# Kernel tuning notes

Measured on AMD Instinct MI355X. Metric: run time of the kernel, lower is better.

Reference implementation:

```python
import jax, jax.numpy as jnp
from jax import lax
import numpy as np

B, T, IN, H, OUT = 64, 512, 128, 512, 1


def _lstm_layer(x, W_ih, W_hh, b_ih, b_hh):
    # x: [B, T, in]; W_ih: [4H, in]; W_hh: [4H, H]; biases: [4H]
    # PyTorch gate order: i, f, g, o
    xg = jnp.einsum('bti,gi->btg', x, W_ih) + (b_ih + b_hh)  # [B, T, 4H]
    Hd = W_hh.shape[1]
    h0 = jnp.zeros((x.shape[0], Hd), x.dtype)

    def step(carry, xt):
        h, c = carry
        g = xt + h @ W_hh.T  # [B, 4H]
        i, f, gg, o = jnp.split(g, 4, axis=-1)
        i = jax.nn.sigmoid(i)
        f = jax.nn.sigmoid(f)
        gg = jnp.tanh(gg)
        o = jax.nn.sigmoid(o)
        c = f * c + i * gg
        h = o * jnp.tanh(c)
        return (h, c), h

    (_, _), hs = lax.scan(step, (h0, h0), jnp.swapaxes(xg, 0, 1))  # hs: [T, B, H]
    return jnp.swapaxes(hs, 0, 1)  # [B, T, H]


def setup_inputs() -> dict:
    key = jax.random.key(0)
    ks = jax.random.split(key, 11)
    s_in = 1.0 / np.sqrt(H)
    inp = {
        'x': jax.random.normal(ks[0], (B, T, IN), jnp.float32),
        'W_ih0': jax.random.uniform(ks[1], (4 * H, IN), jnp.float32, -s_in, s_in),
        'W_hh0': jax.random.uniform(ks[2], (4 * H, H), jnp.float32, -s_in, s_in),
        'b_ih0': jax.random.uniform(ks[3], (4 * H,), jnp.float32, -s_in, s_in),
        'b_hh0': jax.random.uniform(ks[4], (4 * H,), jnp.float32, -s_in, s_in),
        'W_ih1': jax.random.uniform(ks[5], (4 * H, H), jnp.float32, -s_in, s_in),
        'W_hh1': jax.random.uniform(ks[6], (4 * H, H), jnp.float32, -s_in, s_in),
        'b_ih1': jax.random.uniform(ks[7], (4 * H,), jnp.float32, -s_in, s_in),
        'b_hh1': jax.random.uniform(ks[8], (4 * H,), jnp.float32, -s_in, s_in),
        'Wl': jax.random.uniform(ks[9], (OUT, H), jnp.float32, -s_in, s_in),
        'bl': jax.random.uniform(ks[10], (OUT,), jnp.float32, -s_in, s_in),
    }
    return inp


def reference(x, W_ih0, W_hh0, b_ih0, b_hh0, W_ih1, W_hh1, b_ih1, b_hh1, Wl, bl):
    h = _lstm_layer(x, W_ih0, W_hh0, b_ih0, b_hh0)   # layer 0
    h = _lstm_layer(h, W_ih1, W_hh1, b_ih1, b_hh1)   # layer 1
    last = h[:, -1, :]                                # [B, H]
    out = last @ Wl.T + bl                            # [B, OUT]; classification=False -> no sigmoid
    return out
```

## Files before the change

kernel.cpp:

```cpp
#include <hip/hip_runtime.h>
#include <cmath>

#define TT 512
#define BB 64
#define HH 512
#define II 128
#define NBLK 256

typedef float v2f __attribute__((ext_vector_type(2)));
__device__ __forceinline__ v2f fma2(v2f a, v2f b, v2f c) { return __builtin_elementwise_fma(a, b, c); }

#define SMEM_FLOATS (16384 + 16384 + 1024 + 256 + 16)
#define SMEM_BYTES  (SMEM_FLOATS * 4)

__device__ __forceinline__ float sigm(float v) { return 1.0f / (1.0f + expf(-v)); }
__device__ __forceinline__ unsigned umin2(unsigned a, unsigned b) { return a < b ? a : b; }
#define CBAR() asm volatile("" ::: "memory")

__device__ __forceinline__ v2f loadh2(const float* p) {
  unsigned long long r = __hip_atomic_load((const unsigned long long*)p,
                                           __ATOMIC_RELAXED, __HIP_MEMORY_SCOPE_AGENT);
  v2f v;
  v.x = __uint_as_float((unsigned)r);
  v.y = __uint_as_float((unsigned)(r >> 32));
  return v;
}
template<int KN>
__device__ __forceinline__ void loadh2b(const float* __restrict__ src, int k0,
                                        int bp, v2f (&v)[KN]) {
#pragma unroll
  for (int i = 0; i < KN; ++i) v[i] = loadh2(src + (size_t)(k0 + i) * BB + 2 * bp);
}
template<int KN>
__device__ __forceinline__ void loadx2(const float* __restrict__ src, int k0,
                                       int bp, v2f (&v)[KN]) {
#pragma unroll
  for (int i = 0; i < KN; ++i)
    v[i] = *(const v2f*)(src + (size_t)(k0 + i) * BB + 2 * bp);
}

__device__ __forceinline__ void step2(const float* wk8, v2f h2, v2f (&acc)[8]) {
  const float4* wp = (const float4*)wk8;
  const float4 w0 = wp[0], w1 = wp[1];
  acc[0] = fma2((v2f){w0.x, w0.x}, h2, acc[0]);
  acc[1] = fma2((v2f){w0.y, w0.y}, h2, acc[1]);
  acc[2] = fma2((v2f){w0.z, w0.z}, h2, acc[2]);
  acc[3] = fma2((v2f){w0.w, w0.w}, h2, acc[3]);
  acc[4] = fma2((v2f){w1.x, w1.x}, h2, acc[4]);
  acc[5] = fma2((v2f){w1.y, w1.y}, h2, acc[5]);
  acc[6] = fma2((v2f){w1.z, w1.z}, h2, acc[6]);
  acc[7] = fma2((v2f){w1.w, w1.w}, h2, acc[7]);
}
template<int KN>
__device__ __forceinline__ void consume2(const float* __restrict__ wro, int k0,
                                         const v2f (&v)[KN], v2f (&acc)[8]) {
#pragma unroll
  for (int i = 0; i < KN; ++i) step2(wro + (size_t)(k0 + i) * 16, v[i], acc);
}

__device__ __forceinline__ void span32(const float* __restrict__ src,
                                       const float* __restrict__ wro,
                                       int k0, int bp, v2f (&acc)[8]) {
  v2f a[4], b[4];
  loadh2b<4>(src, k0,      bp, a);
  loadh2b<4>(src, k0 + 4,  bp, b);
  consume2<4>(wro, k0,      a, acc);
  loadh2b<4>(src, k0 + 8,  bp, a);
  consume2<4>(wro, k0 + 4,  b, acc);
  loadh2b<4>(src, k0 + 12, bp, b);
  consume2<4>(wro, k0 + 8,  a, acc);
  loadh2b<4>(src, k0 + 16, bp, a);
  consume2<4>(wro, k0 + 12, b, acc);
  loadh2b<4>(src, k0 + 20, bp, b);
  consume2<4>(wro, k0 + 16, a, acc);
  loadh2b<4>(src, k0 + 24, bp, a);
  consume2<4>(wro, k0 + 20, b, acc);
  loadh2b<4>(src, k0 + 28, bp, b);
  consume2<4>(wro, k0 + 24, a, acc);
  consume2<4>(wro, k0 + 28, b, acc);
}

__global__ __launch_bounds__(1024) void k_transpose_x(const float* __restrict__ x,
                                                      float* __restrict__ xT) {
  __shared__ float tile[64][65];
  const int t  = blockIdx.x >> 1;
  const int k0 = (blockIdx.x & 1) << 6;
  const int lk = threadIdx.x & 63;
  const int lb = threadIdx.x >> 6;
#pragma unroll
  for (int bp = 0; bp < 64; bp += 16) {
    const int b = bp + lb;
    tile[lk][b] = x[((size_t)b * TT + t) * II + k0 + lk];
  }
  __syncthreads();
  const int b2  = threadIdx.x & 63;
  const int kk0 = threadIdx.x >> 6;
#pragma unroll
  for (int kp = 0; kp < 64; kp += 16) {
    const int kk = kp + kk0;
    xT[((size_t)t * II + k0 + kk) * BB + b2] = tile[kk][b2];
  }
}

__global__ void k_init_flags(unsigned* flags) { flags[threadIdx.x] = 0u; }

__global__ __launch_bounds__(1024, 4) void k_lstm_persist(
    const float* __restrict__ xT,
    const float* __restrict__ W_ih0, const float* __restrict__ W_hh0,
    const float* __restrict__ b_ih0, const float* __restrict__ b_hh0,
    const float* __restrict__ W_ih1, const float* __restrict__ W_hh1,
    const float* __restrict__ b_ih1, const float* __restrict__ b_hh1,
    float* __restrict__ h0ring, float* __restrict__ h1ring,
    unsigned* __restrict__ flags)
{
  extern __shared__ float smem[];
  float* wlds  = smem;
  float* part  = wlds + 16384;
  float* gates = part + 16384;
  float* cst   = gates + 1024;
  float* bsum  = cst + 256;

  const int bid = blockIdx.x;
  const int L   = bid >> 7;
  const int ub  = (bid & 127) << 2;
  const int tid = threadIdx.x;

  const float* WA = L ? W_ih1 : W_ih0;
  const float* WB = L ? W_hh1 : W_hh0;
  const int KA = L ? HH : II;

  const int ktot = KA + HH;
  for (int idx = tid; idx < 16 * ktot; idx += 1024) {
    const int k  = idx >> 4;
    const int lr = idx & 15;
    const int u = lr >> 2, q = lr & 3;
    const int G = q * HH + ub + u;
    wlds[idx] = (k < KA) ? WA[G * KA + k] : WB[G * HH + (k - KA)];
  }
  if (tid < 16) {
    const int u = tid >> 2, q = tid & 3;
    const int G = q * HH + ub + u;
    bsum[tid] = L ? (b_ih1[G] + b_hh1[G]) : (b_ih0[G] + b_hh0[G]);
  }
  if (tid < 256) cst[tid] = 0.0f;
  __syncthreads();

  const int bp    = tid & 31;
  const int rhalf = (tid >> 5) & 1;
  const int kseg  = tid >> 6;

  const float* wroA = wlds + rhalf * 8;
  const float* wroB0 = wlds + (size_t)II * 16 + rhalf * 8;
  const float* wroB1 = wlds + (size_t)HH * 16 + rhalf * 8;

  for (int s = 0; s <= TT; ++s) {
    const int t = L ? (s - 1) : s;
    const bool active = (t >= 0 && t < TT);
    const bool first  = (t == 0);

    v2f acc[8];
#pragma unroll
    for (int j = 0; j < 8; ++j) acc[j] = (v2f){0.0f, 0.0f};

    v2f xa[4], xb[4];
    if (active && L == 0) {
      const float* xp = xT + (size_t)t * (II * BB);
      loadx2<4>(xp, kseg * 8,     bp, xa);
      loadx2<4>(xp, kseg * 8 + 4, bp, xb);
    }

    if (s > 0) {
      if (tid < 64) {
        const unsigned tgt = (unsigned)s;
        for (;;) {
          const unsigned m0 = __hip_atomic_load(flags + tid,       __ATOMIC_RELAXED, __HIP_MEMORY_SCOPE_AGENT);
          const unsigned m1 = __hip_atomic_load(flags + tid +  64, __ATOMIC_RELAXED, __HIP_MEMORY_SCOPE_AGENT);
          const unsigned m2 = __hip_atomic_load(flags + tid + 128, __ATOMIC_RELAXED, __HIP_MEMORY_SCOPE_AGENT);
          const unsigned m3 = __hip_atomic_load(flags + tid + 192, __ATOMIC_RELAXED, __HIP_MEMORY_SCOPE_AGENT);
          const unsigned mn = umin2(umin2(m0, m1), umin2(m2, m3));
          if (__all(mn >= tgt)) break;
          __builtin_amdgcn_s_sleep(1);
        }
      }
      __syncthreads();
      CBAR();
    }

    if (active) {
      if (L == 0) {
        consume2<4>(wroA, kseg * 8,     xa, acc);
        consume2<4>(wroA, kseg * 8 + 4, xb, acc);
        if (!first) {
          span32(h0ring + (size_t)((s - 1) & 1) * (HH * BB),
                 wroB0, kseg * 32, bp, acc);
        }
      } else {
        span32(h0ring + (size_t)((s - 1) & 1) * (HH * BB),
               wroA, kseg * 32, bp, acc);
        if (!first) {
          span32(h1ring + (size_t)(s & 1) * (HH * BB),
                 wroB1, kseg * 32, bp, acc);
        }
      }

#pragma unroll
      for (int j = 0; j < 8; ++j) {
        const int row = rhalf * 8 + j;
        *(v2f*)(part + ((((size_t)row * 16 + kseg) * 32 + bp) << 1)) = acc[j];
      }
      __syncthreads();
      {
        const int row = tid >> 6;
        const int bb  = tid & 63;
        float g = 0.0f;
#pragma unroll
        for (int ks = 0; ks < 16; ++ks)
          g += part[((((size_t)row * 16 + ks) * 32 + (bb >> 1)) << 1) + (bb & 1)];
        gates[row * 64 + bb] = g + bsum[row];
      }
      __syncthreads();

      if (tid < 256) {
        const int u = tid >> 6, bb = tid & 63;
        const float gi = sigm(gates[((u << 2) + 0) * 64 + bb]);
        const float gf = sigm(gates[((u << 2) + 1) * 64 + bb]);
        const float gg = tanhf(gates[((u << 2) + 2) * 64 + bb]);
        const float go = sigm(gates[((u << 2) + 3) * 64 + bb]);
        const float cold = first ? 0.0f : cst[u * 64 + bb];
        const float cn = gf * cold + gi * gg;
        const float hn = go * tanhf(cn);
        cst[u * 64 + bb] = cn;
        float* hdst = (L ? h1ring : h0ring) + (size_t)(t & 1) * (HH * BB);
        float old = __hip_atomic_exchange(hdst + (ub + u) * 64 + bb, hn,
                                          __ATOMIC_RELAXED, __HIP_MEMORY_SCOPE_AGENT);
        asm volatile("" :: "v"(old));
      }
    }

    __syncthreads();
    if (tid == 0) {
      __hip_atomic_store(flags + bid, (unsigned)(s + 1),
                         __ATOMIC_RELAXED, __HIP_MEMORY_SCOPE_AGENT);
    }
  }
}

__global__ __launch_bounds__(512) void k_final(const float* __restrict__ h1last,
                                               const float* __restrict__ Wl,
                                               const float* __restrict__ bl,
                                               float* __restrict__ out) {
  __shared__ float red[8][64];
  const int jg = threadIdx.x >> 6, b = threadIdx.x & 63;
  float a = 0.0f;
  for (int jj = 0; jj < 64; ++jj) {
    const int j = (jg << 6) + jj;
    a += h1last[j * BB + b] * Wl[j];
  }
  red[jg][b] = a;
  __syncthreads();
  if (threadIdx.x < 64) {
    float s = bl[0];
#pragma unroll
    for (int g = 0; g < 8; ++g) s += red[g][threadIdx.x];
    out[threadIdx.x] = s;
  }
}

extern "C" void kernel_launch(void* const* d_in, const int* in_sizes, int n_in,
                              void* d_out, int out_size, void* d_ws, size_t ws_size,
                              hipStream_t stream) {
  (void)in_sizes; (void)n_in; (void)out_size; (void)ws_size;
  const float* x     = (const float*)d_in[0];
  const float* W_ih0 = (const float*)d_in[1];
  const float* W_hh0 = (const float*)d_in[2];
  const float* b_ih0 = (const float*)d_in[3];
  const float* b_hh0 = (const float*)d_in[4];
  const float* W_ih1 = (const float*)d_in[5];
  const float* W_hh1 = (const float*)d_in[6];
  const float* b_ih1 = (const float*)d_in[7];
  const float* b_hh1 = (const float*)d_in[8];
  const float* Wl    = (const float*)d_in[9];
  const float* bl    = (const float*)d_in[10];
  float* out = (float*)d_out;

  float* ws       = (float*)d_ws;
  float* xT       = ws;
  float* h0ring   = xT + (size_t)TT * II * BB;
  float* h1ring   = h0ring + 2 * HH * BB;
  unsigned* flags = (unsigned*)(h1ring + 2 * HH * BB);

  k_transpose_x<<<1024, 1024, 0, stream>>>(x, xT);
  k_init_flags<<<1, NBLK, 0, stream>>>(flags);

  hipFuncSetAttribute((const void*)k_lstm_persist,
                      hipFuncAttributeMaxDynamicSharedMemorySize, SMEM_BYTES);

  void* args[] = {
    (void*)&xT,
    (void*)&W_ih0, (void*)&W_hh0, (void*)&b_ih0, (void*)&b_hh0,
    (void*)&W_ih1, (void*)&W_hh1, (void*)&b_ih1, (void*)&b_hh1,
    (void*)&h0ring, (void*)&h1ring, (void*)&flags,
  };
  hipLaunchCooperativeKernel((void*)k_lstm_persist, dim3(NBLK), dim3(1024),
                             args, SMEM_BYTES, stream);

  k_final<<<1, 512, 0, stream>>>(h1ring + HH * BB, Wl, bl, out);
}
```

Before: 7.434 ms.

## Overlap input projection with flag spin, fast gate math, packed flag and h exchanges

Moves the layer-0 input-projection FMAs ahead of the inter-block flag wait so they overlap with synchronisation latency. Replaces expf/tanhf with hardware v_exp/v_rcp approximations and applies the activations during the gate reduction, spread over all 1024 threads instead of 256. The flag poll uses 64-bit loads (two flags each), h stores are packed as 64-bit atomic exchanges, and the final flag store is skipped. The fast approximations trade some accuracy, and the final flag skip relies on no consumer waiting for it.

```diff
diff --git a/kernel.cpp b/kernel.cpp
--- a/kernel.cpp
+++ b/kernel.cpp
@@ -13,7 +13,11 @@
 #define SMEM_FLOATS (16384 + 16384 + 1024 + 256 + 16)
 #define SMEM_BYTES  (SMEM_FLOATS * 4)
 
-__device__ __forceinline__ float sigm(float v) { return 1.0f / (1.0f + expf(-v)); }
+__device__ __forceinline__ float fexp2(float x) { float r; asm("v_exp_f32 %0, %1" : "=v"(r) : "v"(x)); return r; }
+__device__ __forceinline__ float frcpf(float x) { float r; asm("v_rcp_f32 %0, %1" : "=v"(r) : "v"(x)); return r; }
+__device__ __forceinline__ float sigm(float v)  { return frcpf(1.0f + fexp2(-1.44269504f * v)); }
+__device__ __forceinline__ float ftanh(float v) { return __builtin_fmaf(2.0f, frcpf(1.0f + fexp2(-2.88539008f * v)), -1.0f); }
+
 __device__ __forceinline__ unsigned umin2(unsigned a, unsigned b) { return a < b ? a : b; }
 #define CBAR() asm volatile("" ::: "memory")
 
@@ -149,7 +153,7 @@
   const int rhalf = (tid >> 5) & 1;
   const int kseg  = tid >> 6;
 
-  const float* wroA = wlds + rhalf * 8;
+  const float* wroA  = wlds + rhalf * 8;
   const float* wroB0 = wlds + (size_t)II * 16 + rhalf * 8;
   const float* wroB1 = wlds + (size_t)HH * 16 + rhalf * 8;
 
@@ -162,22 +166,24 @@
 #pragma unroll
     for (int j = 0; j < 8; ++j) acc[j] = (v2f){0.0f, 0.0f};
 
-    v2f xa[4], xb[4];
     if (active && L == 0) {
+      v2f xa[4], xb[4];
       const float* xp = xT + (size_t)t * (II * BB);
       loadx2<4>(xp, kseg * 8,     bp, xa);
       loadx2<4>(xp, kseg * 8 + 4, bp, xb);
+      consume2<4>(wroA, kseg * 8,     xa, acc);
+      consume2<4>(wroA, kseg * 8 + 4, xb, acc);
     }
 
     if (s > 0) {
       if (tid < 64) {
         const unsigned tgt = (unsigned)s;
+        const unsigned long long* f64 = (const unsigned long long*)flags;
         for (;;) {
-          const unsigned m0 = __hip_atomic_load(flags + tid,       __ATOMIC_RELAXED, __HIP_MEMORY_SCOPE_AGENT);
-          const unsigned m1 = __hip_atomic_load(flags + tid +  64, __ATOMIC_RELAXED, __HIP_MEMORY_SCOPE_AGENT);
-          const unsigned m2 = __hip_atomic_load(flags + tid + 128, __ATOMIC_RELAXED, __HIP_MEMORY_SCOPE_AGENT);
-          const unsigned m3 = __hip_atomic_load(flags + tid + 192, __ATOMIC_RELAXED, __HIP_MEMORY_SCOPE_AGENT);
-          const unsigned mn = umin2(umin2(m0, m1), umin2(m2, m3));
+          const unsigned long long a = __hip_atomic_load(f64 + tid,      __ATOMIC_RELAXED, __HIP_MEMORY_SCOPE_AGENT);
+          const unsigned long long b = __hip_atomic_load(f64 + tid + 64, __ATOMIC_RELAXED, __HIP_MEMORY_SCOPE_AGENT);
+          const unsigned mn = umin2(umin2((unsigned)a, (unsigned)(a >> 32)),
+                                    umin2((unsigned)b, (unsigned)(b >> 32)));
           if (__all(mn >= tgt)) break;
           __builtin_amdgcn_s_sleep(1);
         }
@@ -188,8 +194,6 @@
 
     if (active) {
       if (L == 0) {
-        consume2<4>(wroA, kseg * 8,     xa, acc);
-        consume2<4>(wroA, kseg * 8 + 4, xb, acc);
         if (!first) {
           span32(h0ring + (size_t)((s - 1) & 1) * (HH * BB),
                  wroB0, kseg * 32, bp, acc);
@@ -212,33 +216,48 @@
       {
         const int row = tid >> 6;
         const int bb  = tid & 63;
+        const int q   = row & 3;
         float g = 0.0f;
 #pragma unroll
         for (int ks = 0; ks < 16; ++ks)
           g += part[((((size_t)row * 16 + ks) * 32 + (bb >> 1)) << 1) + (bb & 1)];
-        gates[row * 64 + bb] = g + bsum[row];
+        g += bsum[row];
+        gates[row * 64 + bb] = (q == 2) ? ftanh(g) : sigm(g);
       }
       __syncthreads();
 
-      if (tid < 256) {
-        const int u = tid >> 6, bb = tid & 63;
-        const float gi = sigm(gates[((u << 2) + 0) * 64 + bb]);
-        const float gf = sigm(gates[((u << 2) + 1) * 64 + bb]);
-        const float gg = tanhf(gates[((u << 2) + 2) * 64 + bb]);
-        const float go = sigm(gates[((u << 2) + 3) * 64 + bb]);
-        const float cold = first ? 0.0f : cst[u * 64 + bb];
-        const float cn = gf * cold + gi * gg;
-        const float hn = go * tanhf(cn);
-        cst[u * 64 + bb] = cn;
+      if (tid < 128) {
+        const int u   = tid >> 5;
+        const int bb0 = (tid & 31) << 1, bb1 = bb0 + 1;
+        const float gi0 = gates[((u << 2) + 0) * 64 + bb0];
+        const float gf0 = gates[((u << 2) + 1) * 64 + bb0];
+        const float gg0 = gates[((u << 2) + 2) * 64 + bb0];
+        const float go0 = gates[((u << 2) + 3) * 64 + bb0];
+        const float gi1 = gates[((u << 2) + 0) * 64 + bb1];
+        const float gf1 = gates[((u << 2) + 1) * 64 + bb1];
+        const float gg1 = gates[((u << 2) + 2) * 64 + bb1];
+        const float go1 = gates[((u << 2) + 3) * 64 + bb1];
+        const float c0 = first ? 0.0f : cst[u * 64 + bb0];
+        const float c1 = first ? 0.0f : cst[u * 64 + bb1];
+        const float cn0 = gf0 * c0 + gi0 * gg0;
+        const float cn1 = gf1 * c1 + gi1 * gg1;
+        const float hn0 = go0 * ftanh(cn0);
+        const float hn1 = go1 * ftanh(cn1);
+        cst[u * 64 + bb0] = cn0;
+        cst[u * 64 + bb1] = cn1;
         float* hdst = (L ? h1ring : h0ring) + (size_t)(t & 1) * (HH * BB);
-        float old = __hip_atomic_exchange(hdst + (ub + u) * 64 + bb, hn,
-                                          __ATOMIC_RELAXED, __HIP_MEMORY_SCOPE_AGENT);
+        unsigned long long pk =
+            (unsigned long long)__float_as_uint(hn0) |
+            ((unsigned long long)__float_as_uint(hn1) << 32);
+        unsigned long long old = __hip_atomic_exchange(
+            (unsigned long long*)(hdst + (ub + u) * 64 + bb0), pk,
+            __ATOMIC_RELAXED, __HIP_MEMORY_SCOPE_AGENT);
         asm volatile("" :: "v"(old));
       }
     }
 
     __syncthreads();
-    if (tid == 0) {
+    if (tid == 0 && s < TT) {
       __hip_atomic_store(flags + bid, (unsigned)(s + 1),
                          __ATOMIC_RELAXED, __HIP_MEMORY_SCOPE_AGENT);
     }
```

Measured after the change: 6.953 ms (median of 2 runs). -6.5%, faster.
